# Kernel optimization log

Hardware: AMD Instinct MI355X
Metric: run time of the kernel (lower is better)

## Reference

```python
import jax, jax.numpy as jnp
import numpy as np

N, E = 10000, 160000
D, H, C, FF, L = 128, 4, 32, 512, 2
INNER = H * C
VOCAB, RELVOCAB = 32000, 100
EPS = 1e-6
GATE_BIAS = 3.0


def _layer_norm(x, w, b):
    mu = jnp.mean(x, axis=-1, keepdims=True)
    var = jnp.mean(jnp.square(x - mu), axis=-1, keepdims=True)
    return (x - mu) * jax.lax.rsqrt(var + EPS) * w + b


def setup_inputs() -> dict:
    key = jax.random.key(0)
    ks = jax.random.split(key, 24)
    s = 1.0 / np.sqrt(D)
    inp = {
        "node_ids": jax.random.randint(ks[0], (N,), 0, VOCAB),
        "edge_index": jax.random.randint(ks[1], (2, E), 0, N),
        "edge_ids": jax.random.randint(ks[2], (E,), 0, RELVOCAB),
        "node_emb": jax.random.normal(ks[3], (VOCAB, D), jnp.float32),
        "edge_emb": jax.random.normal(ks[4], (RELVOCAB, D), jnp.float32),
        # per-layer stacked params (torch Linear weight layout [out, in])
        "ln_w": jnp.ones((L, D), jnp.float32),
        "ln_b": jnp.zeros((L, D), jnp.float32),
        "q_w": jax.random.normal(ks[5], (L, INNER, D), jnp.float32) * (1.0 / np.sqrt(D * C)),
        "relA_w": jax.random.normal(ks[6], (L, FF, 2 * D), jnp.float32) * s,
        "relA_b": jnp.zeros((L, FF), jnp.float32),
        "relB_w": jax.random.normal(ks[7], (L, D, FF), jnp.float32) * s,
        "relB_b": jnp.zeros((L, D), jnp.float32),
        "relG_w": jax.random.normal(ks[8], (L, D, FF), jnp.float32) * s,
        "relG_b": jnp.zeros((L, D), jnp.float32),
        "k_w": jax.random.normal(ks[9], (L, INNER, 2 * D), jnp.float32) * s,
        "v_w": jax.random.normal(ks[10], (L, INNER, D), jnp.float32) * s,
        "o_w": jax.random.normal(ks[11], (L, D, INNER), jnp.float32) * (1.0 / np.sqrt(INNER)),
        "ff_ln_w": jnp.ones((L, D), jnp.float32),
        "ff_ln_b": jnp.zeros((L, D), jnp.float32),
        "wi_w": jax.random.normal(ks[12], (L, FF, D), jnp.float32) * s,
        "wo_w": jax.random.normal(ks[13], (L, D, FF), jnp.float32) * (1.0 / np.sqrt(FF)),
    }
    return inp


def _forward(node_ids, edge_index, edge_ids, node_emb, edge_emb, ln_w, ln_b,
             q_w, relA_w, relA_b, relB_w, relB_b, relG_w, relG_b,
             k_w, v_w, o_w, ff_ln_w, ff_ln_b, wi_w, wo_w):
    x = node_emb[node_ids]          # [N, D]
    ef = edge_emb[edge_ids]         # [E, D]
    src = edge_index[0]             # j (source / kv side)
    dst = edge_index[1]             # i (target / query side)
    for l in range(L):
        # --- relational self-attention ---
        q = _layer_norm(x, ln_w[l], ln_b[l])
        q = (q @ q_w[l].T).reshape(N, H, C)
        kv_j = x[src]                                   # [E, D]
        cat = jnp.concatenate([kv_j, ef], axis=-1)      # [E, 2D]
        inter = jax.nn.celu(cat @ relA_w[l].T + relA_b[l])   # [E, FF]
        gate = jax.nn.sigmoid(inter @ relG_w[l].T + relG_b[l] + GATE_BIAS)
        k_add = inter @ relB_w[l].T + relB_b[l]
        kv2 = kv_j * gate + k_add * (1.0 - gate)        # [E, D]
        k = (jnp.concatenate([kv2, ef], axis=-1) @ k_w[l].T).reshape(E, H, C)
        v = (kv2 @ v_w[l].T).reshape(E, H, C)
        scores = jnp.sum(q[dst] * k, axis=-1)           # [E, H]
        smax = jax.ops.segment_max(scores, dst, num_segments=N)
        ex = jnp.exp(scores - smax[dst])
        denom = jax.ops.segment_sum(ex, dst, num_segments=N)
        alpha = ex / denom[dst]                         # [E, H]
        msg = (v * alpha[..., None]).reshape(E, INNER)
        agg = jax.ops.segment_sum(msg, dst, num_segments=N)  # [N, INNER]
        x = x + agg @ o_w[l].T
        # --- feed-forward (T5-style, pre-LN, relu, residual) ---
        h = _layer_norm(x, ff_ln_w[l], ff_ln_b[l])
        x = x + jax.nn.relu(h @ wi_w[l].T) @ wo_w[l].T
    return x


def reference(node_ids, edge_index, edge_ids, node_emb, edge_emb, ln_w, ln_b,
              q_w, relA_w, relA_b, relB_w, relB_b, relG_w, relG_b,
              k_w, v_w, o_w, ff_ln_w, ff_ln_b, wi_w, wo_w):
    return _forward(node_ids, edge_index, edge_ids, node_emb, edge_emb, ln_w, ln_b,
                    q_w, relA_w, relA_b, relB_w, relB_b, relG_w, relG_b,
                    k_w, v_w, o_w, ff_ln_w, ff_ln_b, wi_w, wo_w)
```

## Files before the change

### kernel.cpp

```cpp
#include <hip/hip_runtime.h>
#include <hip/hip_bf16.h>

#define NN 10000
#define EE 160000
#define DD 128
#define HH 4
#define CC 32
#define FFF 512
#define LL 2
#define RELV 100
#define EPS 1e-6f
#define GATE_BIAS 3.0f
#define BM 32
#define NT 16

typedef __bf16 bf16x8 __attribute__((ext_vector_type(8)));
typedef float f32x4 __attribute__((ext_vector_type(4)));
typedef float f32x16 __attribute__((ext_vector_type(16)));

#define MFMA(a,b,c)   __builtin_amdgcn_mfma_f32_16x16x32_bf16((a),(b),(c),0,0,0)
#define MFMA32(a,b,c) __builtin_amdgcn_mfma_f32_32x32x16_bf16((a),(b),(c),0,0,0)

__device__ __forceinline__ int swzK(int e, int b){ return e*256 + (b ^ ((e&7)<<4)); }
__device__ __forceinline__ int swzI(int e, int b){ return e*512 + (b ^ ((e&7)<<4)); }
__device__ __forceinline__ int swz128(int e, int b){ return e*256 + (b ^ ((e&7)<<4)); }
__device__ __forceinline__ int swz512(int e, int b){ return e*1024 + (b ^ ((e&7)<<4)); }

__global__ __launch_bounds__(256) void k_gx(
    const int* __restrict__ node_ids, const float* __restrict__ node_emb,
    float* __restrict__ x, ushort* __restrict__ xb,
    const int* __restrict__ dst, int* __restrict__ hist){
  int b = blockIdx.x, t = threadIdx.x;
  int n = b*2 + (t>>7);
  int c = t & 127;
  float v = node_emb[(long)node_ids[n]*DD + c];
  x[(long)n*DD + c] = v;
  __hip_bfloat16 h = __float2bfloat16(v);
  xb[(long)n*DD + c] = *(ushort*)&h;
  if (t < 32){
    int e = b*32 + t;
    atomicAdd(&hist[dst[e]], 1);
  }
}

__device__ __forceinline__ void wprep_one(
    const float* __restrict__ in, ushort* __restrict__ out, int tid, int IN, int instride){
  int lane = tid & 63;
  int grp  = tid >> 6;
  int nkb  = IN >> 4;
  int kb   = grp % nkb;
  int cb   = grp / nkb;
  int col  = cb*32 + (lane & 31);
  int k0   = kb*16 + (lane >> 5)*8;
  const float* p = in + (long)col*instride + k0;
  bf16x8 h;
  #pragma unroll
  for (int j=0;j<8;++j) h[j] = (__bf16)p[j];
  *(bf16x8*)(out + (long)tid*8) = h;
}

__global__ __launch_bounds__(256) void k_prep2(
    const float* __restrict__ relG_w, const float* __restrict__ relB_w,
    const float* __restrict__ k_w, const float* __restrict__ v_w,
    const float* __restrict__ relA_w,
    const float* __restrict__ q_w, const float* __restrict__ o_w,
    const float* __restrict__ wi_w, const float* __restrict__ wo_w,
    ushort* __restrict__ Gwb, ushort* __restrict__ Bwb,
    ushort* __restrict__ Kwb, ushort* __restrict__ Vwb, ushort* __restrict__ A1b,
    ushort* __restrict__ Qwb, ushort* __restrict__ Owb,
    ushort* __restrict__ Wib, ushort* __restrict__ Wob){
  const int bid = blockIdx.x;
  const int l   = bid >> 8;
  const int tidl = (bid & 255)*256 + threadIdx.x;
  const long gid = (long)bid*256 + threadIdx.x;
  if (tidl < DD*FFF/8){
    wprep_one(relG_w + (long)l*DD*FFF, Gwb + (long)l*DD*FFF, tidl, FFF, FFF);
    wprep_one(relB_w + (long)l*DD*FFF, Bwb + (long)l*DD*FFF, tidl, FFF, FFF);
  }
  if (tidl < DD*DD/8){
    wprep_one(k_w + (long)l*DD*256, Kwb + (long)l*DD*DD, tidl, DD, 256);
    wprep_one(v_w + (long)l*DD*DD,  Vwb + (long)l*DD*DD, tidl, DD, DD);
  }
  {
    int o = tidl / DD, i = tidl % DD;
    __hip_bfloat16 h = __float2bfloat16(relA_w[(long)l*FFF*256 + (long)o*256 + i]);
    A1b[(long)l*FFF*DD + tidl] = *(ushort*)&h;
  }
  if (gid < (long)LL*DD*DD){
    __hip_bfloat16 h1 = __float2bfloat16(q_w[gid]); Qwb[gid] = *(ushort*)&h1;
    __hip_bfloat16 h2 = __float2bfloat16(o_w[gid]); Owb[gid] = *(ushort*)&h2;
  }
  {
    __hip_bfloat16 h3 = __float2bfloat16(wi_w[gid]); Wib[gid] = *(ushort*)&h3;
    __hip_bfloat16 h4 = __float2bfloat16(wo_w[gid]); Wob[gid] = *(ushort*)&h4;
  }
}

__global__ __launch_bounds__(256) void k_ea2(
    const float* __restrict__ edge_emb, const float* __restrict__ relA_w,
    const float* __restrict__ relA_b, const float* __restrict__ k_w,
    ushort* __restrict__ EA2b, float* __restrict__ EKf){
  int l = blockIdx.x / RELV, rel = blockIdx.x % RELV, t = threadIdx.x;
  const float* Aw = relA_w + (long)l*FFF*256;
  const float* Ab = relA_b + (long)l*FFF;
  const float* Kw = k_w + (long)l*DD*256;
  ushort* EAo = EA2b + (long)l*RELV*FFF;
  float* EKo  = EKf + (long)l*RELV*DD;
  __shared__ float emb[128];
  if (t < 128) emb[t] = edge_emb[(long)rel*DD + t];
  __syncthreads();
  for (int f=t; f<FFF; f+=256){
    const float* wr = Aw + (long)f*256 + 128;
    float s = Ab[f];
    for (int i=0;i<128;++i) s += emb[i]*wr[i];
    __hip_bfloat16 h = __float2bfloat16(s);
    EAo[(long)rel*FFF + f] = *(ushort*)&h;
  }
  if (t < 128){
    const float* wr = Kw + (long)t*256 + 128;
    float s = 0.f;
    for (int i=0;i<128;++i) s += emb[i]*wr[i];
    EKo[(long)rel*DD + t] = s;
  }
}

__global__ __launch_bounds__(256) void k_scan(const int* __restrict__ hist, int* __restrict__ cursor){
  __shared__ int tsum[256];
  const int t = threadIdx.x;
  const int PER = (NN + 255) / 256;
  const int base = t*PER;
  int s = 0;
  for (int i=0;i<PER;++i){ int idx = base+i; if (idx < NN) s += hist[idx]; }
  tsum[t] = s;
  __syncthreads();
  if (t == 0){
    int run = 0;
    for (int i=0;i<256;++i){ int v = tsum[i]; tsum[i] = run; run += v; }
  }
  __syncthreads();
  int run = tsum[t];
  for (int i=0;i<PER;++i){
    int idx = base+i;
    if (idx < NN){ int v = hist[idx]; cursor[idx] = run; run += v; }
  }
}
__global__ __launch_bounds__(256) void k_scatter(const int* __restrict__ dst,
    int* __restrict__ cursor, int* __restrict__ perm){
  int e = blockIdx.x*256 + threadIdx.x;
  if (e < EE){
    int p = atomicAdd(&cursor[dst[e]], 1);
    perm[p] = e;
  }
}

__global__ __launch_bounds__(256) void k_lnq_xa(
    const float* __restrict__ x, const float* __restrict__ lnw, const float* __restrict__ lnb,
    const ushort* __restrict__ qwb, const ushort* __restrict__ a1b,
    float* __restrict__ q, ushort* __restrict__ XAb,
    float* __restrict__ agg, float* __restrict__ denom){
  __shared__ __align__(16) unsigned char HB[NT*256];
  __shared__ __align__(16) unsigned char HR[NT*256];
  const int n0 = blockIdx.x*NT;
  const int t = threadIdx.x;
  const int e = t>>4, s = t&15;
  const int w = t>>6, l = t&63, lr = l&15, lg = l>>4;
  {
    float4 z4 = {0.f,0.f,0.f,0.f};
    float* ap = agg + (long)n0*DD + t*8;
    *(float4*)ap = z4; *(float4*)(ap+4) = z4;
    if (t < NT*HH) denom[n0*HH + t] = 0.f;
  }
  {
    const float* xp = x + (long)(n0+e)*DD + s*8;
    float xv[8];
    *(float4*)&xv[0] = *(const float4*)xp;
    *(float4*)&xv[4] = *(const float4*)(xp+4);
    float sm = 0.f;
    #pragma unroll
    for (int i=0;i<8;++i) sm += xv[i];
    sm += __shfl_xor(sm,1); sm += __shfl_xor(sm,2);
    sm += __shfl_xor(sm,4); sm += __shfl_xor(sm,8);
    float mu = sm*(1.f/DD);
    float sq = 0.f;
    #pragma unroll
    for (int i=0;i<8;++i){ float d = xv[i]-mu; sq += d*d; }
    sq += __shfl_xor(sq,1); sq += __shfl_xor(sq,2);
    sq += __shfl_xor(sq,4); sq += __shfl_xor(sq,8);
    float rstd = rsqrtf(sq*(1.f/DD) + EPS);
    float4 w0 = *(const float4*)(lnw + s*8), w1 = *(const float4*)(lnw + s*8 + 4);
    float4 b0 = *(const float4*)(lnb + s*8), b1 = *(const float4*)(lnb + s*8 + 4);
    float wv[8] = {w0.x,w0.y,w0.z,w0.w,w1.x,w1.y,w1.z,w1.w};
    float bv[8] = {b0.x,b0.y,b0.z,b0.w,b1.x,b1.y,b1.z,b1.w};
    bf16x8 hb, hr;
    #pragma unroll
    for (int i=0;i<8;++i){
      hb[i] = (__bf16)((xv[i]-mu)*rstd*wv[i] + bv[i]);
      hr[i] = (__bf16)xv[i];
    }
    *(bf16x8*)(HB + swz128(e, s*16)) = hb;
    *(bf16x8*)(HR + swz128(e, s*16)) = hr;
  }
  __syncthreads();
  {
    const int o0 = w*32;
    f32x4 z = {0.f,0.f,0.f,0.f};
    f32x4 acc[2] = {z,z};
    #pragma unroll
    for (int k4=0;k4<4;++k4){
      bf16x8 a = *(const bf16x8*)(HB + swz128(lr, k4*64 + lg*16));
      #pragma unroll
      for (int nt=0;nt<2;++nt){
        bf16x8 b = *(const bf16x8*)(qwb + (long)(o0+nt*16+lr)*128 + k4*32 + lg*8);
        acc[nt] = MFMA(a, b, acc[nt]);
      }
    }
    #pragma unroll
    for (int nt=0;nt<2;++nt)
      #pragma unroll
      for (int r=0;r<4;++r)
        q[(long)(n0 + lg*4 + r)*DD + o0 + nt*16 + lr] = acc[nt][r];
  }
  {
    const int f0w = w*128;
    f32x4 z = {0.f,0.f,0.f,0.f};
    f32x4 acc[8] = {z,z,z,z,z,z,z,z};
    #pragma unroll
    for (int k4=0;k4<4;++k4){
      bf16x8 a = *(const bf16x8*)(HR + swz128(lr, k4*64 + lg*16));
      #pragma unroll
      for (int nt=0;nt<8;++nt){
        bf16x8 b = *(const bf16x8*)(a1b + (long)(f0w+nt*16+lr)*128 + k4*32 + lg*8);
        acc[nt] = MFMA(a, b, acc[nt]);
      }
    }
    #pragma unroll
    for (int nt=0;nt<8;++nt)
      #pragma unroll
      for (int r=0;r<4;++r){
        __hip_bfloat16 h = __float2bfloat16(acc[nt][r]);
        XAb[(long)(n0+lg*4+r)*FFF + f0w+nt*16+lr] = *(ushort*)&h;
      }
  }
}

__global__ __launch_bounds__(256,4) void k_edge(
    const ushort* __restrict__ xb, const ushort* __restrict__ XAb,
    const ushort* __restrict__ EAb, const float* __restrict__ EKf,
    const float* __restrict__ q,
    const int* __restrict__ src, const int* __restrict__ dst, const int* __restrict__ eids,
    const int* __restrict__ perm,
    const ushort* __restrict__ Gwb, const float* __restrict__ Gb,
    const ushort* __restrict__ Bwb, const float* __restrict__ Bb,
    const ushort* __restrict__ Kwb, const ushort* __restrict__ Vwb,
    float* __restrict__ agg, float* __restrict__ denom)
{
  __shared__ __align__(16) unsigned char KVB[BM*256];
  __shared__ __align__(16) unsigned char INTB[BM*512];
  __shared__ int srcl[BM], dstl[BM], eidl[BM];

  int nb;
  {
    const int cpx = (EE/BM) >> 3;
    nb = (blockIdx.x & 7)*cpx + (blockIdx.x >> 3);
  }
  const int e0 = nb * BM;
  const int t  = threadIdx.x;
  const int w  = t >> 6;
  const int l  = t & 63;
  const int c32 = l & 31;
  const int hi  = l >> 5;
  const int C = w;
  const int oc = C*32 + c32;

  if (t < BM){
    int pe = perm[e0+t];
    srcl[t] = src[pe]; dstl[t] = dst[pe]; eidl[t] = eids[pe];
  }
  __syncthreads();

  {
    const uint4* xbu = (const uint4*)xb;
    #pragma unroll
    for (int it=0; it<2; ++it){
      int g = it*256 + t;
      int e = g >> 4, qq = g & 15;
      *(uint4*)(KVB + swzK(e, qq*16)) = xbu[(long)srcl[e]*16 + qq];
    }
  }

  f32x16 gbG, gbB;
  {
    float bg = Gb[oc] + GATE_BIAS;
    float bb = Bb[oc];
    #pragma unroll
    for (int i=0;i<16;++i){ gbG[i] = bg; gbB[i] = bb; }
  }

  bf16x8 xa8[4], ea8[4];
  #pragma unroll
  for (int it=0; it<4; ++it){
    int g = it*256 + t;
    int e = g >> 5, c8 = g & 31;
    xa8[it] = *(const bf16x8*)(XAb + (long)srcl[e]*FFF + c8*8);
    ea8[it] = *(const bf16x8*)(EAb + (long)eidl[e]*FFF + c8*8);
  }

  #pragma unroll
  for (int ch=0; ch<2; ++ch){
    #pragma unroll
    for (int it=0; it<4; ++it){
      bf16x8 o;
      #pragma unroll
      for (int j=0;j<8;++j){
        float s = (float)xa8[it][j] + (float)ea8[it][j];
        o[j] = (__bf16)((s > 0.f) ? s : (__expf(s) - 1.f));
      }
      int g = it*256 + t;
      int e = g >> 5, c8 = g & 31;
      *(bf16x8*)(INTB + swzI(e, c8*16)) = o;
    }
    __syncthreads();
    if (ch == 0){
      #pragma unroll
      for (int it=0; it<4; ++it){
        int g = it*256 + t;
        int e = g >> 5, c8 = g & 31;
        xa8[it] = *(const bf16x8*)(XAb + (long)srcl[e]*FFF + 256 + c8*8);
        ea8[it] = *(const bf16x8*)(EAb + (long)eidl[e]*FFF + 256 + c8*8);
      }
    }
    {
      const ushort* Wg = Gwb + ((long)(C*32 + ch*16)*64 + l)*8;
      #pragma unroll
      for (int h2=0; h2<2; ++h2){
        bf16x8 wf[8];
        #pragma unroll
        for (int i=0;i<8;++i) wf[i] = *(const bf16x8*)(Wg + (long)(h2*8+i)*512);
        #pragma unroll
        for (int i=0;i<8;++i){
          bf16x8 a = *(const bf16x8*)(INTB + swzI(c32, (h2*8+i)*32 + hi*16));
          gbG = MFMA32(a, wf[i], gbG);
        }
      }
    }
    {
      const ushort* Wb = Bwb + ((long)(C*32 + ch*16)*64 + l)*8;
      #pragma unroll
      for (int h2=0; h2<2; ++h2){
        bf16x8 wf[8];
        #pragma unroll
        for (int i=0;i<8;++i) wf[i] = *(const bf16x8*)(Wb + (long)(h2*8+i)*512);
        #pragma unroll
        for (int i=0;i<8;++i){
          bf16x8 a = *(const bf16x8*)(INTB + swzI(c32, (h2*8+i)*32 + hi*16));
          gbB = MFMA32(a, wf[i], gbB);
        }
      }
    }
    if (ch == 0) __syncthreads();
  }

  #pragma unroll
  for (int r=0;r<16;++r){
    int row = (r&3) + 8*(r>>2) + 4*hi;
    float g  = 1.f/(1.f + __expf(-gbG[r]));
    float kv = (float)*(const __bf16*)(KVB + swzK(row, oc*2));
    float k2 = gbB[r] + g*(kv - gbB[r]);
    *(__bf16*)(KVB + swzK(row, oc*2)) = (__bf16)k2;
  }
  __syncthreads();

  f32x16 ka, va;
  #pragma unroll
  for (int i=0;i<16;++i){ ka[i] = 0.f; va[i] = 0.f; }
  {
    const ushort* Wk = Kwb + ((long)(C*8)*64 + l)*8;
    bf16x8 wf[8];
    #pragma unroll
    for (int i=0;i<8;++i) wf[i] = *(const bf16x8*)(Wk + (long)i*512);
    #pragma unroll
    for (int i=0;i<8;++i){
      bf16x8 a = *(const bf16x8*)(KVB + swzK(c32, i*32 + hi*16));
      ka = MFMA32(a, wf[i], ka);
    }
  }
  {
    const ushort* Wv = Vwb + ((long)(C*8)*64 + l)*8;
    bf16x8 wf[8];
    #pragma unroll
    for (int i=0;i<8;++i) wf[i] = *(const bf16x8*)(Wv + (long)i*512);
    #pragma unroll
    for (int i=0;i<8;++i){
      bf16x8 a = *(const bf16x8*)(KVB + swzK(c32, i*32 + hi*16));
      va = MFMA32(a, wf[i], va);
    }
  }

  #pragma unroll
  for (int qq=0; qq<4; ++qq){
    const int base = 8*qq + 4*hi;
    float ex[4];
    #pragma unroll
    for (int j=0;j<4;++j){
      int r = qq*4 + j;
      int gr = base + j;
      float kv = ka[r] + EKf[(long)eidl[gr]*DD + oc];
      float p = kv * q[(long)dstl[gr]*DD + oc];
      p += __shfl_xor(p, 1); p += __shfl_xor(p, 2);
      p += __shfl_xor(p, 4); p += __shfl_xor(p, 8);
      p += __shfl_xor(p, 16);
      ex[j] = __expf(p);
    }
    {
      float acc = va[qq*4]*ex[0];
      int cur = dstl[base];
      #pragma unroll
      for (int j=1;j<4;++j){
        int dn = dstl[base+j];
        if (dn != cur){
          atomicAdd(&agg[(long)cur*DD + oc], acc);
          acc = 0.f; cur = dn;
        }
        acc += va[qq*4+j]*ex[j];
      }
      atomicAdd(&agg[(long)cur*DD + oc], acc);
    }
    if (c32 == 0){
      float da = ex[0];
      int cur = dstl[base];
      #pragma unroll
      for (int j=1;j<4;++j){
        int dn = dstl[base+j];
        if (dn != cur){
          atomicAdd(&denom[cur*HH + C], da);
          da = 0.f; cur = dn;
        }
        da += ex[j];
      }
      atomicAdd(&denom[cur*HH + C], da);
    }
  }
}

template<bool FUSE_LNQ>
__global__ __launch_bounds__(256) void k_node(
    const float* __restrict__ agg, const float* __restrict__ denom,
    const ushort* __restrict__ owb,
    const float* __restrict__ lnw, const float* __restrict__ lnb,
    const ushort* __restrict__ wib, const ushort* __restrict__ wob,
    float* __restrict__ x, ushort* __restrict__ xb,
    const float* __restrict__ nlnw, const float* __restrict__ nlnb,
    const ushort* __restrict__ nqwb, const ushort* __restrict__ na1b,
    float* __restrict__ q, ushort* __restrict__ XAb){
  __shared__ __align__(16) unsigned char AB[NT*256];
  __shared__ __align__(16) unsigned char IB[NT*1024];
  __shared__ __align__(16) float XO[NT][132];
  const int n0 = blockIdx.x*NT;
  const int t = threadIdx.x;
  const int e = t>>4, s = t&15;
  const int w = t>>6, l = t&63, lr = l&15, lg = l>>4;

  {
    const float* ap = agg + (long)(n0+e)*DD + s*8;
    float av[8];
    *(float4*)&av[0] = *(const float4*)ap;
    *(float4*)&av[4] = *(const float4*)(ap+4);
    float dinv = 1.f / denom[(n0+e)*HH + (s>>2)];
    bf16x8 hb;
    #pragma unroll
    for (int i=0;i<8;++i) hb[i] = (__bf16)(av[i]*dinv);
    *(bf16x8*)(AB + swz128(e, s*16)) = hb;
  }
  __syncthreads();

  {
    const int o0 = w*32;
    f32x4 z = {0.f,0.f,0.f,0.f};
    f32x4 acc[2] = {z,z};
    #pragma unroll
    for (int k4=0;k4<4;++k4){
      bf16x8 a = *(const bf16x8*)(AB + swz128(lr, k4*64 + lg*16));
      #pragma unroll
      for (int nt=0;nt<2;++nt){
        bf16x8 b = *(const bf16x8*)(owb + (long)(o0+nt*16+lr)*128 + k4*32 + lg*8);
        acc[nt] = MFMA(a, b, acc[nt]);
      }
    }
    #pragma unroll
    for (int nt=0;nt<2;++nt)
      #pragma unroll
      for (int r=0;r<4;++r)
        XO[lg*4+r][o0+nt*16+lr] = acc[nt][r];
  }
  __syncthreads();

  float x1[8];
  {
    const float* xp = x + (long)(n0+e)*DD + s*8;
    float xv[8];
    *(float4*)&xv[0] = *(const float4*)xp;
    *(float4*)&xv[4] = *(const float4*)(xp+4);
    #pragma unroll
    for (int i=0;i<8;++i) x1[i] = xv[i] + XO[e][s*8+i];
    float sm = 0.f;
    #pragma unroll
    for (int i=0;i<8;++i) sm += x1[i];
    sm += __shfl_xor(sm,1); sm += __shfl_xor(sm,2);
    sm += __shfl_xor(sm,4); sm += __shfl_xor(sm,8);
    float mu = sm*(1.f/DD);
    float sq = 0.f;
    #pragma unroll
    for (int i=0;i<8;++i){ float d = x1[i]-mu; sq += d*d; }
    sq += __shfl_xor(sq,1); sq += __shfl_xor(sq,2);
    sq += __shfl_xor(sq,4); sq += __shfl_xor(sq,8);
    float rstd = rsqrtf(sq*(1.f/DD) + EPS);
    float4 w0 = *(const float4*)(lnw + s*8), w1 = *(const float4*)(lnw + s*8 + 4);
    float4 b0 = *(const float4*)(lnb + s*8), b1 = *(const float4*)(lnb + s*8 + 4);
    float wv[8] = {w0.x,w0.y,w0.z,w0.w,w1.x,w1.y,w1.z,w1.w};
    float bv[8] = {b0.x,b0.y,b0.z,b0.w,b1.x,b1.y,b1.z,b1.w};
    bf16x8 hb;
    #pragma unroll
    for (int i=0;i<8;++i) hb[i] = (__bf16)((x1[i]-mu)*rstd*wv[i] + bv[i]);
    __syncthreads();
    *(bf16x8*)(AB + swz128(e, s*16)) = hb;
  }
  __syncthreads();

  {
    const int f0w = w*128;
    f32x4 z = {0.f,0.f,0.f,0.f};
    f32x4 acc[8] = {z,z,z,z,z,z,z,z};
    #pragma unroll
    for (int k4=0;k4<4;++k4){
      bf16x8 a = *(const bf16x8*)(AB + swz128(lr, k4*64 + lg*16));
      #pragma unroll
      for (int nt=0;nt<8;++nt){
        bf16x8 b = *(const bf16x8*)(wib + (long)(f0w+nt*16+lr)*128 + k4*32 + lg*8);
        acc[nt] = MFMA(a, b, acc[nt]);
      }
    }
    #pragma unroll
    for (int nt=0;nt<8;++nt)
      #pragma unroll
      for (int r=0;r<4;++r){
        int e2 = lg*4 + r;
        int f = f0w + nt*16 + lr;
        float va = acc[nt][r];
        *(__bf16*)(IB + swz512(e2, f*2)) = (__bf16)fmaxf(va, 0.f);
      }
  }
  __syncthreads();

  {
    const int o0 = w*32;
    f32x4 z = {0.f,0.f,0.f,0.f};
    f32x4 acc[2] = {z,z};
    #pragma unroll
    for (int k16=0;k16<16;++k16){
      bf16x8 a = *(const bf16x8*)(IB + swz512(lr, k16*64 + lg*16));
      #pragma unroll
      for (int nt=0;nt<2;++nt){
        bf16x8 b = *(const bf16x8*)(wob + (long)(o0+nt*16+lr)*512 + k16*32 + lg*8);
        acc[nt] = MFMA(a, b, acc[nt]);
      }
    }
    #pragma unroll
    for (int nt=0;nt<2;++nt)
      #pragma unroll
      for (int r=0;r<4;++r)
        XO[lg*4+r][o0+nt*16+lr] = acc[nt][r];
  }
  __syncthreads();

  float xn[8];
  {
    #pragma unroll
    for (int i=0;i<8;++i) xn[i] = x1[i] + XO[e][s*8+i];
    float* xp = x + (long)(n0+e)*DD + s*8;
    *(float4*)xp = *(float4*)&xn[0];
    *(float4*)(xp+4) = *(float4*)&xn[4];
    bf16x8 hb;
    #pragma unroll
    for (int i=0;i<8;++i) hb[i] = (__bf16)xn[i];
    *(bf16x8*)(xb + (long)(n0+e)*DD + s*8) = hb;
  }

  if constexpr (FUSE_LNQ){
    {
      float4 z4 = {0.f,0.f,0.f,0.f};
      float* ap = (float*)agg + (long)n0*DD + t*8;
      *(float4*)ap = z4; *(float4*)(ap+4) = z4;
      if (t < NT*HH) ((float*)denom)[n0*HH + t] = 0.f;
    }
    {
      float sm = 0.f;
      #pragma unroll
      for (int i=0;i<8;++i) sm += xn[i];
      sm += __shfl_xor(sm,1); sm += __shfl_xor(sm,2);
      sm += __shfl_xor(sm,4); sm += __shfl_xor(sm,8);
      float mu = sm*(1.f/DD);
      float sq = 0.f;
      #pragma unroll
      for (int i=0;i<8;++i){ float d = xn[i]-mu; sq += d*d; }
      sq += __shfl_xor(sq,1); sq += __shfl_xor(sq,2);
      sq += __shfl_xor(sq,4); sq += __shfl_xor(sq,8);
      float rstd = rsqrtf(sq*(1.f/DD) + EPS);
      float4 w0 = *(const float4*)(nlnw + s*8), w1 = *(const float4*)(nlnw + s*8 + 4);
      float4 b0 = *(const float4*)(nlnb + s*8), b1 = *(const float4*)(nlnb + s*8 + 4);
      float wv[8] = {w0.x,w0.y,w0.z,w0.w,w1.x,w1.y,w1.z,w1.w};
      float bv[8] = {b0.x,b0.y,b0.z,b0.w,b1.x,b1.y,b1.z,b1.w};
      bf16x8 hb, hr;
      #pragma unroll
      for (int i=0;i<8;++i){
        hb[i] = (__bf16)((xn[i]-mu)*rstd*wv[i] + bv[i]);
        hr[i] = (__bf16)xn[i];
      }
      *(bf16x8*)(AB + swz128(e, s*16)) = hb;
      *(bf16x8*)(IB + swz128(e, s*16)) = hr;
    }
    __syncthreads();
    {
      const int o0 = w*32;
      f32x4 z = {0.f,0.f,0.f,0.f};
      f32x4 acc[2] = {z,z};
      #pragma unroll
      for (int k4=0;k4<4;++k4){
        bf16x8 a = *(const bf16x8*)(AB + swz128(lr, k4*64 + lg*16));
        #pragma unroll
        for (int nt=0;nt<2;++nt){
          bf16x8 b = *(const bf16x8*)(nqwb + (long)(o0+nt*16+lr)*128 + k4*32 + lg*8);
          acc[nt] = MFMA(a, b, acc[nt]);
        }
      }
      #pragma unroll
      for (int nt=0;nt<2;++nt)
        #pragma unroll
        for (int r=0;r<4;++r)
          q[(long)(n0 + lg*4 + r)*DD + o0 + nt*16 + lr] = acc[nt][r];
    }
    {
      const int f0w = w*128;
      f32x4 z = {0.f,0.f,0.f,0.f};
      f32x4 acc[8] = {z,z,z,z,z,z,z,z};
      #pragma unroll
      for (int k4=0;k4<4;++k4){
        bf16x8 a = *(const bf16x8*)(IB + swz128(lr, k4*64 + lg*16));
        #pragma unroll
        for (int nt=0;nt<8;++nt){
          bf16x8 b = *(const bf16x8*)(na1b + (long)(f0w+nt*16+lr)*128 + k4*32 + lg*8);
          acc[nt] = MFMA(a, b, acc[nt]);
        }
      }
      #pragma unroll
      for (int nt=0;nt<8;++nt)
        #pragma unroll
        for (int r=0;r<4;++r){
          __hip_bfloat16 h = __float2bfloat16(acc[nt][r]);
          XAb[(long)(n0+lg*4+r)*FFF + f0w+nt*16+lr] = *(ushort*)&h;
        }
    }
  }
}

extern "C" void kernel_launch(void* const* d_in, const int* in_sizes, int n_in,
                              void* d_out, int out_size, void* d_ws, size_t ws_size,
                              hipStream_t stream) {
  const int* node_ids   = (const int*)d_in[0];
  const int* edge_index = (const int*)d_in[1];
  const int* edge_ids   = (const int*)d_in[2];
  const float* node_emb = (const float*)d_in[3];
  const float* edge_emb = (const float*)d_in[4];
  const float* ln_w   = (const float*)d_in[5];
  const float* ln_b   = (const float*)d_in[6];
  const float* q_w    = (const float*)d_in[7];
  const float* relA_w = (const float*)d_in[8];
  const float* relA_b = (const float*)d_in[9];
  const float* relB_w = (const float*)d_in[10];
  const float* relB_b = (const float*)d_in[11];
  const float* relG_w = (const float*)d_in[12];
  const float* relG_b = (const float*)d_in[13];
  const float* k_w    = (const float*)d_in[14];
  const float* v_w    = (const float*)d_in[15];
  const float* o_w    = (const float*)d_in[16];
  const float* ff_ln_w= (const float*)d_in[17];
  const float* ff_ln_b= (const float*)d_in[18];
  const float* wi_w   = (const float*)d_in[19];
  const float* wo_w   = (const float*)d_in[20];
  const int* src = edge_index;
  const int* dst = edge_index + EE;

  float* ws = (float*)d_ws;
  float* x   = ws;  ws += (long)NN*DD;
  float* q   = ws;  ws += (long)NN*DD;
  float* denom = ws; ws += NN*HH;
  float* agg   = ws; ws += (long)NN*DD;
  float* EKf   = ws; ws += (long)LL*RELV*DD;
  int* hist   = (int*)ws; ws += NN;
  int* perm   = (int*)ws; ws += EE;
  ushort* xb  = (ushort*)ws; ws += (long)NN*DD/2;
  ushort* XAb = (ushort*)ws; ws += (long)NN*FFF/2;
  ushort* EAb = (ushort*)ws; ws += (long)LL*RELV*FFF/2;
  ushort* A1b = (ushort*)ws; ws += (long)LL*FFF*DD/2;
  ushort* Gwb = (ushort*)ws; ws += (long)LL*DD*FFF/2;
  ushort* Bwb = (ushort*)ws; ws += (long)LL*DD*FFF/2;
  ushort* Kwb = (ushort*)ws; ws += (long)LL*DD*DD/2;
  ushort* Vwb = (ushort*)ws; ws += (long)LL*DD*DD/2;
  ushort* Qwb = (ushort*)ws; ws += (long)LL*DD*DD/2;
  ushort* Owb = (ushort*)ws; ws += (long)LL*DD*DD/2;
  ushort* Wib = (ushort*)ws; ws += (long)LL*FFF*DD/2;
  ushort* Wob = (ushort*)ws; ws += (long)LL*DD*FFF/2;

  hipMemsetAsync(hist, 0, NN*sizeof(int), stream);
  k_gx<<<NN/2, 256, 0, stream>>>(node_ids, node_emb, x, xb, dst, hist);
  k_scan<<<1, 256, 0, stream>>>(hist, hist);
  k_scatter<<<(EE+255)/256, 256, 0, stream>>>(dst, hist, perm);
  k_prep2<<<512, 256, 0, stream>>>(relG_w, relB_w, k_w, v_w, relA_w,
                                   q_w, o_w, wi_w, wo_w,
                                   Gwb, Bwb, Kwb, Vwb, A1b, Qwb, Owb, Wib, Wob);
  k_ea2<<<2*RELV, 256, 0, stream>>>(edge_emb, relA_w, relA_b, k_w, EAb, EKf);

  k_lnq_xa<<<NN/NT, 256, 0, stream>>>(x, ln_w, ln_b, Qwb, A1b, q, XAb, agg, denom);
  for (int l=0; l<LL; ++l){
    k_edge<<<EE/BM, 256, 0, stream>>>(xb, XAb, EAb + (long)l*RELV*FFF, EKf + (long)l*RELV*DD,
        q, src, dst, edge_ids, perm,
        Gwb + (long)l*DD*FFF,  relG_b + (long)l*DD,
        Bwb + (long)l*DD*FFF,  relB_b + (long)l*DD,
        Kwb + (long)l*DD*DD,   Vwb + (long)l*DD*DD,
        agg, denom);
    if (l < LL-1){
      k_node<true><<<NN/NT, 256, 0, stream>>>(agg, denom, Owb + (long)l*DD*DD,
          ff_ln_w + l*DD, ff_ln_b + l*DD,
          Wib + (long)l*FFF*DD, Wob + (long)l*DD*FFF, x, xb,
          ln_w + (l+1)*DD, ln_b + (l+1)*DD,
          Qwb + (long)(l+1)*DD*DD, A1b + (long)(l+1)*FFF*DD, q, XAb);
    } else {
      k_node<false><<<NN/NT, 256, 0, stream>>>(agg, denom, Owb + (long)l*DD*DD,
          ff_ln_w + l*DD, ff_ln_b + l*DD,
          Wib + (long)l*FFF*DD, Wob + (long)l*DD*FFF, x, xb,
          nullptr, nullptr, nullptr, nullptr, nullptr, nullptr);
    }
  }
  hipMemcpyAsync(d_out, x, (size_t)NN*DD*sizeof(float), hipMemcpyDeviceToDevice, stream);
}
```

Baseline: 421.0 us.

## Double-buffer intermediate activations in four 128-wide chunks in edge kernel

```diff
diff --git a/kernel.cpp b/kernel.cpp
--- a/kernel.cpp
+++ b/kernel.cpp
@@ -22,7 +22,6 @@
 #define MFMA32(a,b,c) __builtin_amdgcn_mfma_f32_32x32x16_bf16((a),(b),(c),0,0,0)
 
 __device__ __forceinline__ int swzK(int e, int b){ return e*256 + (b ^ ((e&7)<<4)); }
-__device__ __forceinline__ int swzI(int e, int b){ return e*512 + (b ^ ((e&7)<<4)); }
 __device__ __forceinline__ int swz128(int e, int b){ return e*256 + (b ^ ((e&7)<<4)); }
 __device__ __forceinline__ int swz512(int e, int b){ return e*1024 + (b ^ ((e&7)<<4)); }
 
@@ -255,7 +254,7 @@
     float* __restrict__ agg, float* __restrict__ denom)
 {
   __shared__ __align__(16) unsigned char KVB[BM*256];
-  __shared__ __align__(16) unsigned char INTB[BM*512];
+  __shared__ __align__(16) unsigned char INTB[2][BM*256];
   __shared__ int srcl[BM], dstl[BM], eidl[BM];
 
   int nb;
@@ -296,68 +295,65 @@
     for (int i=0;i<16;++i){ gbG[i] = bg; gbB[i] = bb; }
   }
 
-  bf16x8 xa8[4], ea8[4];
+  bf16x8 xa8[2], ea8[2];
   #pragma unroll
-  for (int it=0; it<4; ++it){
+  for (int it=0; it<2; ++it){
     int g = it*256 + t;
-    int e = g >> 5, c8 = g & 31;
+    int e = g >> 4, c8 = g & 15;
     xa8[it] = *(const bf16x8*)(XAb + (long)srcl[e]*FFF + c8*8);
     ea8[it] = *(const bf16x8*)(EAb + (long)eidl[e]*FFF + c8*8);
   }
 
   #pragma unroll
-  for (int ch=0; ch<2; ++ch){
-    #pragma unroll
-    for (int it=0; it<4; ++it){
-      bf16x8 o;
+  for (int ch=0; ch<4; ++ch){
+    bf16x8 o[2];
+    #pragma unroll
+    for (int it=0; it<2; ++it){
       #pragma unroll
       for (int j=0;j<8;++j){
         float s = (float)xa8[it][j] + (float)ea8[it][j];
-        o[j] = (__bf16)((s > 0.f) ? s : (__expf(s) - 1.f));
-      }
+        o[it][j] = (__bf16)((s > 0.f) ? s : (__expf(s) - 1.f));
+      }
+    }
+    unsigned char* INTp = INTB[ch & 1];
+    #pragma unroll
+    for (int it=0; it<2; ++it){
       int g = it*256 + t;
-      int e = g >> 5, c8 = g & 31;
-      *(bf16x8*)(INTB + swzI(e, c8*16)) = o;
+      int e = g >> 4, c8 = g & 15;
+      *(bf16x8*)(INTp + swzK(e, c8*16)) = o[it];
     }
     __syncthreads();
-    if (ch == 0){
-      #pragma unroll
-      for (int it=0; it<4; ++it){
+    if (ch < 3){
+      #pragma unroll
+      for (int it=0; it<2; ++it){
         int g = it*256 + t;
-        int e = g >> 5, c8 = g & 31;
-        xa8[it] = *(const bf16x8*)(XAb + (long)srcl[e]*FFF + 256 + c8*8);
-        ea8[it] = *(const bf16x8*)(EAb + (long)eidl[e]*FFF + 256 + c8*8);
+        int e = g >> 4, c8 = g & 15;
+        xa8[it] = *(const bf16x8*)(XAb + (long)srcl[e]*FFF + (ch+1)*128 + c8*8);
+        ea8[it] = *(const bf16x8*)(EAb + (long)eidl[e]*FFF + (ch+1)*128 + c8*8);
       }
     }
     {
-      const ushort* Wg = Gwb + ((long)(C*32 + ch*16)*64 + l)*8;
-      #pragma unroll
-      for (int h2=0; h2<2; ++h2){
-        bf16x8 wf[8];
-        #pragma unroll
-        for (int i=0;i<8;++i) wf[i] = *(const bf16x8*)(Wg + (long)(h2*8+i)*512);
-        #pragma unroll
-        for (int i=0;i<8;++i){
-          bf16x8 a = *(const bf16x8*)(INTB + swzI(c32, (h2*8+i)*32 + hi*16));
-          gbG = MFMA32(a, wf[i], gbG);
-        }
+      const ushort* Wg = Gwb + ((long)(C*32 + ch*8)*64 + l)*8;
+      bf16x8 wf[8];
+      #pragma unroll
+      for (int i=0;i<8;++i) wf[i] = *(const bf16x8*)(Wg + (long)i*512);
+      #pragma unroll
+      for (int i=0;i<8;++i){
+        bf16x8 a = *(const bf16x8*)(INTp + swzK(c32, i*32 + hi*16));
+        gbG = MFMA32(a, wf[i], gbG);
       }
     }
     {
-      const ushort* Wb = Bwb + ((long)(C*32 + ch*16)*64 + l)*8;
-      #pragma unroll
-      for (int h2=0; h2<2; ++h2){
-        bf16x8 wf[8];
-        #pragma unroll
-        for (int i=0;i<8;++i) wf[i] = *(const bf16x8*)(Wb + (long)(h2*8+i)*512);
-        #pragma unroll
-        for (int i=0;i<8;++i){
-          bf16x8 a = *(const bf16x8*)(INTB + swzI(c32, (h2*8+i)*32 + hi*16));
-          gbB = MFMA32(a, wf[i], gbB);
-        }
-      }
-    }
-    if (ch == 0) __syncthreads();
+      const ushort* Wb = Bwb + ((long)(C*32 + ch*8)*64 + l)*8;
+      bf16x8 wf[8];
+      #pragma unroll
+      for (int i=0;i<8;++i) wf[i] = *(const bf16x8*)(Wb + (long)i*512);
+      #pragma unroll
+      for (int i=0;i<8;++i){
+        bf16x8 a = *(const bf16x8*)(INTp + swzK(c32, i*32 + hi*16));
+        gbB = MFMA32(a, wf[i], gbB);
+      }
+    }
   }
 
   #pragma unroll
```

Result: faster. 411.3 us (-2.3%).
